# Optimization experiments

Hardware: AMD Instinct MI355X
Metric: run time of the kernel (lower is better)

Reference implementation:

```python
import jax, jax.numpy as jnp
from jax import lax
import numpy as np

MAXMAG = 10.0   # max_residue_magnitude
DG = 16         # deformable_groups
K = 9           # 3x3 kernel taps


def _conv(x, w, b):
    return lax.conv_general_dilated(x, w, (1, 1), 'SAME',
                                    dimension_numbers=('NCHW', 'OIHW', 'NCHW')) + b[None, :, None, None]


def _lrelu(v):
    return jnp.where(v >= 0, v, 0.1 * v)


def _sample(img, py, px):
    # img [C,H,W]; py,px [K,H,W] absolute sample coords; bilinear, zeros outside (torchvision semantics)
    H, W = img.shape[1], img.shape[2]
    y0 = jnp.floor(py)
    x0 = jnp.floor(px)
    wy1 = py - y0
    wx1 = px - x0

    def gather(yi, xi):
        valid = ((yi >= 0) & (yi < H) & (xi >= 0) & (xi < W)).astype(img.dtype)
        yc = jnp.clip(yi, 0, H - 1).astype(jnp.int32)
        xc = jnp.clip(xi, 0, W - 1).astype(jnp.int32)
        return img[:, yc, xc] * valid[None]  # [C,K,H,W]

    v00 = gather(y0, x0)
    v01 = gather(y0, x0 + 1)
    v10 = gather(y0 + 1, x0)
    v11 = gather(y0 + 1, x0 + 1)
    return (v00 * ((1 - wy1) * (1 - wx1))[None] + v01 * ((1 - wy1) * wx1)[None]
            + v10 * (wy1 * (1 - wx1))[None] + v11 * (wy1 * wx1)[None])


def setup_inputs() -> dict:
    key = jax.random.key(0)
    ks = jax.random.split(key, 12)
    N, CIN, COUT, H, W = 4, 128, 64, 96, 96
    f = lambda k, sh, s: jax.random.normal(k, sh, dtype=jnp.float32) * s
    return {
        'x': f(ks[0], (N, CIN, H, W), 1.0),
        'extra_feat': f(ks[1], (N, 3 * COUT, H, W), 1.0),
        'flow_1': f(ks[2], (N, 2, H, W), 2.0),
        'flow_2': f(ks[3], (N, 2, H, W), 2.0),
        'w_off0': f(ks[4], (COUT, 3 * COUT + 4, 3, 3), 0.02), 'b_off0': jnp.zeros((COUT,), jnp.float32),
        'w_off1': f(ks[5], (COUT, COUT, 3, 3), 0.04), 'b_off1': jnp.zeros((COUT,), jnp.float32),
        'w_off2': f(ks[6], (COUT, COUT, 3, 3), 0.04), 'b_off2': jnp.zeros((COUT,), jnp.float32),
        'w_off3': f(ks[7], (27 * DG, COUT, 3, 3), 0.02), 'b_off3': jnp.zeros((27 * DG,), jnp.float32),
        'w_dcn': f(ks[8], (COUT, CIN, 3, 3), 0.03), 'b_dcn': jnp.zeros((COUT,), jnp.float32),
    }


def reference(x, extra_feat, flow_1, flow_2, w_off0, b_off0, w_off1, b_off1,
              w_off2, b_off2, w_off3, b_off3, w_dcn, b_dcn):
    N, CIN, H, W = x.shape
    COUT = w_dcn.shape[0]
    Cg = CIN // DG
    # conv_offset stack on cat([extra_feat, flow_1, flow_2])
    feat = jnp.concatenate([extra_feat, flow_1, flow_2], axis=1)
    h = _lrelu(_conv(feat, w_off0, b_off0))
    h = _lrelu(_conv(h, w_off1, b_off1))
    h = _lrelu(_conv(h, w_off2, b_off2))
    out = _conv(h, w_off3, b_off3)                      # [N, 27*DG, H, W]
    o1, o2, mask = jnp.split(out, 3, axis=1)            # each [N, 9*DG, H, W]
    offs = MAXMAG * jnp.tanh(jnp.concatenate([o1, o2], axis=1))
    off1, off2 = jnp.split(offs, 2, axis=1)
    # flow.flip(1) -> (dy, dx); repeat interleaves over the 72 (tap) pairs
    off1 = off1 + jnp.tile(flow_1[:, ::-1], (1, off1.shape[1] // 2, 1, 1))
    off2 = off2 + jnp.tile(flow_2[:, ::-1], (1, off2.shape[1] // 2, 1, 1))
    # torchvision layout: channel c = g*2*K + 2*k + {y,x}; groups 0..7 <- off1, 8..15 <- off2
    off = jnp.concatenate([off1, off2], axis=1).reshape(N, DG, K, 2, H, W)
    m = jax.nn.sigmoid(mask).reshape(N, DG, K, H, W)
    # absolute sampling positions per tap
    kk = jnp.arange(K)
    ky = (kk // 3 - 1).astype(x.dtype)[:, None, None]
    kx = (kk % 3 - 1).astype(x.dtype)[:, None, None]
    gy = jnp.arange(H, dtype=x.dtype)[:, None]
    gx = jnp.arange(W, dtype=x.dtype)[None, :]
    py = off[:, :, :, 0] + ky + gy                      # [N,DG,K,H,W]
    px = off[:, :, :, 1] + kx + gx
    xg = x.reshape(N, DG, Cg, H, W)
    sampled = jax.vmap(jax.vmap(_sample))(xg, py, px)   # [N,DG,Cg,K,H,W]
    wg = w_dcn.reshape(COUT, DG, Cg, K)
    y = jnp.einsum('ngckhw,ogck->nohw', sampled * m[:, :, None], wg)
    return y + b_dcn[None, :, None, None]
```

## Files before the change

kernel.cpp:

```cpp
#include <hip/hip_runtime.h>
#include <math.h>

#define NB 4
#define HH 96
#define WW 96
#define HW (HH*WW)
#define NPIX (NB*HW)
#define C_IN 128
#define C_OUT 64
#define DGRP 16
#define CG 8

typedef short v8s __attribute__((ext_vector_type(8)));
typedef float v4f __attribute__((ext_vector_type(4)));
typedef unsigned short u16;
typedef unsigned int u32;

__device__ __forceinline__ u16 f2bf(float x) {
    u32 u = __float_as_uint(x);
    u32 r = (u + 0x7FFFu + ((u >> 16) & 1u)) >> 16;
    return (u16)r;
}
__device__ __forceinline__ float bf2f(u16 h) {
    return __uint_as_float(((u32)h) << 16);
}
__device__ __forceinline__ float lo_bf(u32 w) { return __uint_as_float(w << 16); }
__device__ __forceinline__ float hi_bf(u32 w) { return __uint_as_float(w & 0xFFFF0000u); }
__device__ __forceinline__ float ftanh(float x) {
    float e = __expf(2.0f * x);
    return 1.0f - 2.0f / (e + 1.0f);
}
__device__ __forceinline__ float fsigm(float x) {
    return 1.0f / (1.0f + __expf(-x));
}
__device__ __forceinline__ v8s u4_to_v8s(uint4 q) {
    union { uint4 q; v8s s; } u; u.q = q; return u.s;
}
__device__ __forceinline__ u32 cvtpk(float a, float b) {
    u32 r;
    asm("v_cvt_pk_bf16_f32 %0, %1, %2" : "=v"(r) : "v"(a), "v"(b));
    return r;
}
typedef __attribute__((address_space(1))) const char gch1;
typedef __attribute__((address_space(3))) char ch3;
__device__ __forceinline__ void gload16(const void* g, void* l) {
    __builtin_amdgcn_global_load_lds((gch1*)g, (ch3*)l, 16, 0, 0);
}

__global__ __launch_bounds__(256) void prep_catT(
    const float* __restrict__ ef, const float* __restrict__ f1,
    const float* __restrict__ f2, u16* __restrict__ catT)
{
    __shared__ float T[64][65];
    const int t   = threadIdx.x;
    const int p   = blockIdx.x * 64;
    const int ch0 = blockIdx.y * 64;
    const int n   = p / HW;
    const int rem = p - n * HW;
    const int px  = t & 63;
    const int wv  = t >> 6;
    #pragma unroll
    for (int kk = 0; kk < 16; ++kk) {
        int chl = wv * 16 + kk;
        int ch  = ch0 + chl;
        float v = 0.f;
        if (ch < 192)      v = ef[(size_t)(n * 192 + ch) * HW + rem + px];
        else if (ch < 194) v = f1[(size_t)(n * 2 + (ch - 192)) * HW + rem + px];
        else if (ch < 196) v = f2[(size_t)(n * 2 + (ch - 194)) * HW + rem + px];
        T[chl][px] = v;
    }
    __syncthreads();
    const int s = t & 7;
    #pragma unroll
    for (int it = 0; it < 2; ++it) {
        int pxo = (t >> 3) + it * 32;
        u32 w0 = (u32)f2bf(T[s*8+0][pxo]) | ((u32)f2bf(T[s*8+1][pxo]) << 16);
        u32 w1 = (u32)f2bf(T[s*8+2][pxo]) | ((u32)f2bf(T[s*8+3][pxo]) << 16);
        u32 w2 = (u32)f2bf(T[s*8+4][pxo]) | ((u32)f2bf(T[s*8+5][pxo]) << 16);
        u32 w3 = (u32)f2bf(T[s*8+6][pxo]) | ((u32)f2bf(T[s*8+7][pxo]) << 16);
        *(uint4*)&catT[((size_t)(p + pxo)) * 256 + ch0 + s * 8] = make_uint4(w0, w1, w2, w3);
    }
}

__global__ __launch_bounds__(256) void prep_xT(
    const float* __restrict__ x, u16* __restrict__ xT)
{
    __shared__ float T[64][65];
    const int t   = threadIdx.x;
    const int p   = blockIdx.x * 64;
    const int ch0 = blockIdx.y * 64;
    const int n   = p / HW;
    const int rem = p - n * HW;
    const int px  = t & 63;
    const int wv  = t >> 6;
    #pragma unroll
    for (int kk = 0; kk < 16; ++kk) {
        int chl = wv * 16 + kk;
        T[chl][px] = x[(size_t)(n * C_IN + ch0 + chl) * HW + rem + px];
    }
    __syncthreads();
    const int s = t & 7;
    #pragma unroll
    for (int it = 0; it < 2; ++it) {
        int pxo = (t >> 3) + it * 32;
        u32 w0 = (u32)f2bf(T[s*8+0][pxo]) | ((u32)f2bf(T[s*8+1][pxo]) << 16);
        u32 w1 = (u32)f2bf(T[s*8+2][pxo]) | ((u32)f2bf(T[s*8+3][pxo]) << 16);
        u32 w2 = (u32)f2bf(T[s*8+4][pxo]) | ((u32)f2bf(T[s*8+5][pxo]) << 16);
        u32 w3 = (u32)f2bf(T[s*8+6][pxo]) | ((u32)f2bf(T[s*8+7][pxo]) << 16);
        *(uint4*)&xT[((size_t)(ch0 / 8 + s) * NPIX + (p + pxo)) * 8] = make_uint4(w0, w1, w2, w3);
    }
}

__device__ __forceinline__ void pack_wf_one(
    const float* __restrict__ w, u16* __restrict__ wp,
    int Cout, int CoutPad, int CIN, int CIP, int idx)
{
    const int NKF = CIP / 32, NOG = CoutPad / 16;
    int c    = idx & 7;
    int ln   = (idx >> 3) & 63;
    int rest = idx >> 9;
    int og   = rest % NOG; rest /= NOG;
    int kfg  = rest % NKF;
    int tap  = rest / NKF;
    int l15 = ln & 15, lg = ln >> 4;
    int o  = og * 16 + l15;
    int ci = kfg * 32 + lg * 8 + c;
    float v = (o < Cout && ci < CIN) ? w[((size_t)o * CIN + ci) * 9 + tap] : 0.f;
    wp[idx] = f2bf(v);
}

__global__ __launch_bounds__(256) void pack_all(
    const float* __restrict__ w0, u16* __restrict__ w0p,
    const float* __restrict__ w1, u16* __restrict__ w1p,
    const float* __restrict__ w2, u16* __restrict__ w2p,
    const float* __restrict__ w3, u16* __restrict__ w3p,
    const float* __restrict__ wd, u16* __restrict__ wdf,
    uint4* __restrict__ zp)
{
    if (blockIdx.x == 0 && threadIdx.x < 32)
        zp[threadIdx.x] = make_uint4(0u, 0u, 0u, 0u);
    int idx = blockIdx.x * 256 + threadIdx.x;
    if (idx < 147456) { pack_wf_one(w0, w0p, 64, 64, 196, 256, idx); return; }
    idx -= 147456;
    if (idx < 36864)  { pack_wf_one(w1, w1p, 64, 64, 64, 64, idx); return; }
    idx -= 36864;
    if (idx < 36864)  { pack_wf_one(w2, w2p, 64, 64, 64, 64, idx); return; }
    idx -= 36864;
    if (idx < 258048) { pack_wf_one(w3, w3p, 432, 448, 64, 64, idx); return; }
    idx -= 258048;
    {
        int c  = idx & 7;
        int ln = (idx >> 3) & 63;
        int m  = (idx >> 9) & 3;
        int kk = idx >> 11;
        int l15 = ln & 15, lg = ln >> 4;
        int o = m * 16 + l15;
        int slot = kk * 4 + lg;
        int g = slot / 9, kt = slot - 9 * g;
        wdf[idx] = f2bf(wd[((size_t)(o * C_IN + g * CG + c)) * 9 + kt]);
    }
}

template<int CIP, int NCHUNK, int OST, bool LRELU, bool TOUT, int NOB>
__global__ __launch_bounds__(256) void conv_mfma(
    const u16* __restrict__ inT,
    const u16* __restrict__ wp,
    const float* __restrict__ bias,
    int CoutReal,
    u16* __restrict__ outT,
    u32* __restrict__ pairT,
    u16* __restrict__ maskT,
    const char* __restrict__ zpc)
{
    constexpr int COLS  = (NOB > 1) ? 100 : 50;
    constexpr int LTILE = 3 * COLS * 64;
    constexpr int LTILE_PAD = (NOB == 1) ? LTILE + 128 : LTILE;
    constexpr int LSZ   = (NCHUNK > 1) ? 2 * LTILE_PAD : LTILE_PAD;
    constexpr int NKF   = CIP / 32;
    constexpr int NOG   = OST / 16;
    __shared__ __align__(16) u16 L[LSZ];

    const int t   = threadIdx.x;
    const int tb  = blockIdx.x;
    const int row = (NOB > 1) ? tb : (tb >> 1);
    const int p0  = (NOB > 1) ? 0 : (tb & 1) * 48;
    const int n   = row / HH;
    const int h   = row - n * HH;
    const int ln  = t & 63;
    const int wv  = t >> 6;
    const int l15 = ln & 15;
    const int lg  = ln >> 4;

    auto stage = [&](int ch, int buf) {
        const int cb = ch * 64;
        const int NCOL = (NOB > 1) ? 98 : 50;
        const int NTASK = 3 * NCOL * 8;
        u16* Lb = &L[buf * LTILE_PAD];
        #pragma unroll
        for (int it = 0; it < (NTASK + 255) / 256; ++it) {
            int task = it * 256 + t;
            if (task < NTASK) {
                int s  = task & 7;
                int cl = task >> 3;
                int r3 = cl / NCOL;
                int c  = cl - r3 * NCOL;
                int yy = h + r3 - 1;
                int xx = p0 + c - 1;
                uint4 v = make_uint4(0u, 0u, 0u, 0u);
                if ((unsigned)yy < HH && (unsigned)xx < WW)
                    v = *(const uint4*)&inT[((size_t)(n * HW + yy * WW + xx)) * CIP + cb + s * 8];
                *(uint4*)&Lb[(r3 * COLS + c) * 64 + ((s ^ (c & 7)) * 8)] = v;
            }
        }
    };

    if constexpr (NOB == 1) {
        const char* inTc = (const char*)inT;
        auto mk = [&](int it) -> const char* {
            int task = it * 256 + t;
            if (task >= 1200) return zpc;
            int s  = task & 7;
            int cl = task >> 3;
            int r3 = cl / 50;
            int c  = cl - r3 * 50;
            int yy = h + r3 - 1;
            int xx = p0 + c - 1;
            bool v = ((unsigned)yy < HH) && ((unsigned)xx < WW);
            int sp = s ^ (c & 7);
            u32 off = ((u32)(n * HW + yy * WW + xx) * (u32)CIP + (u32)(sp * 8)) * 2u;
            return v ? inTc + off : zpc;
        };
        const char* pb0 = mk(0);
        const char* pb1 = mk(1);
        const char* pb2 = mk(2);
        const char* pb3 = mk(3);
        const char* pb4 = mk(4);

        auto gstage = [&](int ch, int buf) {
            u16* Lb = &L[buf * LTILE_PAD];
            const u32 cb2 = (u32)ch * 128u;
            gload16(pb0 + cb2, &Lb[(u32)(0 * 256 + t) * 8u]);
            gload16(pb1 + cb2, &Lb[(u32)(1 * 256 + t) * 8u]);
            gload16(pb2 + cb2, &Lb[(u32)(2 * 256 + t) * 8u]);
            gload16(pb3 + cb2, &Lb[(u32)(3 * 256 + t) * 8u]);
            if (4 * 256 + t < 1200)
                gload16(pb4 + cb2, &Lb[(u32)(4 * 256 + t) * 8u]);
        };

        v4f acc[3];
        #pragma unroll
        for (int i = 0; i < 3; ++i) acc[i] = (v4f){0.f, 0.f, 0.f, 0.f};

        gstage(0, 0);
        for (int ch = 0; ch < NCHUNK; ++ch) {
            __syncthreads();
            if (ch + 1 < NCHUNK) gstage(ch + 1, (ch + 1) & 1);
            const u16* Lb = &L[(ch & 1) * LTILE_PAD];
            #pragma unroll
            for (int tap = 0; tap < 9; ++tap) {
                const int ty = tap / 3, tx = tap - ty * 3;
                #pragma unroll
                for (int kf = 0; kf < 2; ++kf) {
                    v8s b = *(const v8s*)&wp[((((size_t)tap * NKF + (ch * 2 + kf)) * NOG + wv) * 64 + ln) * 8];
                    #pragma unroll
                    for (int fm = 0; fm < 3; ++fm) {
                        int c = fm * 16 + l15 + tx;
                        v8s a = *(const v8s*)&Lb[(ty * COLS + c) * 64 + (((kf * 4 + lg) ^ (c & 7)) * 8)];
                        acc[fm] = __builtin_amdgcn_mfma_f32_16x16x32_bf16(a, b, acc[fm], 0, 0, 0);
                    }
                }
            }
        }

        int o = wv * 16 + l15;
        float bv = (o < CoutReal) ? bias[o] : 0.f;
        #pragma unroll
        for (int fm = 0; fm < 3; ++fm) {
            #pragma unroll
            for (int r = 0; r < 4; ++r) {
                int px = p0 + fm * 16 + lg * 4 + r;
                float v = acc[fm][r] + bv;
                if (LRELU) v = (v >= 0.f) ? v : 0.1f * v;
                outT[((size_t)(n * HW + h * WW + px)) * OST + o] = f2bf(v);
            }
        }
    } else {
        stage(0, 0);
        __syncthreads();
        const size_t gpix = (size_t)n * HW + h * WW;
        const int ob_lo = blockIdx.y * 4;
        const int ob_hi = (ob_lo + 4 < NOB) ? ob_lo + 4 : NOB;

        for (int ob = ob_lo; ob < ob_hi; ++ob) {
            const int obase = ob * 64 + wv * 16;
            if (obase >= 432) continue;

            v4f acc[6];
            #pragma unroll
            for (int i = 0; i < 6; ++i) acc[i] = (v4f){0.f, 0.f, 0.f, 0.f};

            #pragma unroll
            for (int tap = 0; tap < 9; ++tap) {
                const int ty = tap / 3, tx = tap - ty * 3;
                #pragma unroll
                for (int kf = 0; kf < 2; ++kf) {
                    v8s bw = *(const v8s*)&wp[((((size_t)tap * NKF + kf) * NOG + (ob * 4 + wv)) * 64 + ln) * 8];
                    #pragma unroll
                    for (int fm = 0; fm < 6; ++fm) {
                        int c = fm * 16 + l15 + tx;
                        v8s a = *(const v8s*)&L[(ty * COLS + c) * 64 + (((kf * 4 + lg) ^ (c & 7)) * 8)];
                        acc[fm] = __builtin_amdgcn_mfma_f32_16x16x32_bf16(bw, a, acc[fm], 0, 0, 0);
                    }
                }
            }

            float bv[4];
            #pragma unroll
            for (int r = 0; r < 4; ++r) bv[r] = bias[obase + lg * 4 + r];

            if (obase < 288) {
                const int pr = (obase + lg * 4) >> 1;
                #pragma unroll
                for (int fm = 0; fm < 6; ++fm) {
                    const size_t pix = gpix + fm * 16 + l15;
                    u32 v0 = (u32)f2bf(acc[fm][0] + bv[0]) | ((u32)f2bf(acc[fm][1] + bv[1]) << 16);
                    u32 v1 = (u32)f2bf(acc[fm][2] + bv[2]) | ((u32)f2bf(acc[fm][3] + bv[3]) << 16);
                    pairT[(size_t)pr * NPIX + pix]       = v0;
                    pairT[(size_t)(pr + 1) * NPIX + pix] = v1;
                }
            } else {
                #pragma unroll
                for (int fm = 0; fm < 6; ++fm) {
                    const size_t pix = gpix + fm * 16 + l15;
                    #pragma unroll
                    for (int r = 0; r < 4; ++r) {
                        int mch = obase + lg * 4 + r - 288;
                        maskT[(size_t)mch * NPIX + pix] = f2bf(acc[fm][r] + bv[r]);
                    }
                }
            }
        }
    }
}

__global__ __launch_bounds__(384) void dcn_fused(
    const u16* __restrict__ xT,
    const float* __restrict__ f1,
    const float* __restrict__ f2,
    const u32*  __restrict__ pairT,
    const u16*  __restrict__ maskT,
    const u16*  __restrict__ wdf,
    const float* __restrict__ bdcn,
    float* __restrict__ y)
{
    __shared__ __align__(16) v4f R[2][4][128];

    const int t    = threadIdx.x;
    const int xb   = blockIdx.x;
    const int xw   = (xb & 7) * 144 + (xb >> 3);
    const int p0   = xw * 32;
    const int w6   = t >> 6;
    const int ks   = w6 >> 1;
    const int wvs  = w6 & 1;
    const int ln   = t & 63;
    const int l15  = ln & 15;
    const int lg   = ln >> 4;
    const int ts   = wvs * 64 + ln;
    const int n    = p0 / HW;
    const int rem0 = p0 - n * HW;
    const int p    = p0 + wvs * 16 + l15;
    const int rem  = rem0 + wvs * 16 + l15;
    const int h    = rem / WW;
    const int w    = rem - h * WW;

    const char* pTc = (const char*)pairT;
    const char* mTc = (const char*)maskT;
    const char* xTc = (const char*)xT;
    const u32 p4   = (u32)p << 2;
    const u32 p2   = (u32)p << 1;
    const u32 nb16 = (u32)(n * HW) << 4;

    const float f1yh = f1[(size_t)(n * 2 + 1) * HW + rem] + (float)h;
    const float f1xw = f1[(size_t)(n * 2 + 0) * HW + rem] + (float)w;
    const float f2yh = f2[(size_t)(n * 2 + 1) * HW + rem] + (float)h;
    const float f2xw = f2[(size_t)(n * 2 + 0) * HW + rem] + (float)w;

    auto scal = [&](int sl, u32& yx, float& mr) {
        yx = *(const u32*)(pTc + ((u32)sl * (u32)(NPIX * 4) + p4));
        mr = bf2f(*(const u16*)(mTc + ((u32)sl * (u32)(NPIX * 2) + p2)));
    };

    auto coords = [&](int sl, u32 yx, float mr,
                      uint4& q00, uint4& q01, uint4& q10, uint4& q11,
                      float& w00, float& w01, float& w10, float& w11) {
        const int g  = (sl * 57) >> 9;
        const int kt = sl - 9 * g;
        const int ky = (kt * 11) >> 5;
        const int kx = kt - 3 * ky;
        const float fy = (g < 8) ? f1yh : f2yh;
        const float fx = (g < 8) ? f1xw : f2xw;
        const float py  = 10.0f * ftanh(lo_bf(yx)) + (fy + (float)(ky - 1));
        const float pxx = 10.0f * ftanh(hi_bf(yx)) + (fx + (float)(kx - 1));
        const float m   = fsigm(mr);

        const float y0f = floorf(py), x0f = floorf(pxx);
        const int   iy0 = (int)y0f,   ix0 = (int)x0f;
        const float wy = py - y0f, wx = pxx - x0f;
        const bool v0y = ((unsigned)iy0 < HH);
        const bool v1y = ((unsigned)(iy0 + 1) < HH);
        const bool v0x = ((unsigned)ix0 < WW);
        const bool v1x = ((unsigned)(ix0 + 1) < WW);
        const float wy0m = (1.0f - wy) * m, wy1m = wy * m;
        w00 = (v0y && v0x) ? wy0m * (1.0f - wx) : 0.0f;
        w01 = (v0y && v1x) ? wy0m * wx          : 0.0f;
        w10 = (v1y && v0x) ? wy1m * (1.0f - wx) : 0.0f;
        w11 = (v1y && v1x) ? wy1m * wx          : 0.0f;

        const int iy0c = min(max(iy0, 0), HH - 1);
        const int iy1c = min(max(iy0 + 1, 0), HH - 1);
        const int ix0c = min(max(ix0, 0), WW - 1);
        const int ix1c = min(max(ix0 + 1, 0), WW - 1);
        const u32 gof = (u32)g * (u32)(NPIX * 16) + nb16;
        const u32 r0  = gof + (u32)iy0c * (u32)(WW * 16);
        const u32 r1  = gof + (u32)iy1c * (u32)(WW * 16);
        const u32 c0  = (u32)ix0c << 4;
        const u32 c1  = (u32)ix1c << 4;
        q00 = *(const uint4*)(xTc + (r0 + c0));
        q01 = *(const uint4*)(xTc + (r0 + c1));
        q10 = *(const uint4*)(xTc + (r1 + c0));
        q11 = *(const uint4*)(xTc + (r1 + c1));
    };

    auto blend = [&](const uint4& q00, const uint4& q01,
                     const uint4& q10, const uint4& q11,
                     float w00, float w01, float w10, float w11) -> v8s {
        u32 pv0 = cvtpk(
            w00*lo_bf(q00.x) + w01*lo_bf(q01.x) + w10*lo_bf(q10.x) + w11*lo_bf(q11.x),
            w00*hi_bf(q00.x) + w01*hi_bf(q01.x) + w10*hi_bf(q10.x) + w11*hi_bf(q11.x));
        u32 pv1 = cvtpk(
            w00*lo_bf(q00.y) + w01*lo_bf(q01.y) + w10*lo_bf(q10.y) + w11*lo_bf(q11.y),
            w00*hi_bf(q00.y) + w01*hi_bf(q01.y) + w10*hi_bf(q10.y) + w11*hi_bf(q11.y));
        u32 pv2 = cvtpk(
            w00*lo_bf(q00.z) + w01*lo_bf(q01.z) + w10*lo_bf(q10.z) + w11*lo_bf(q11.z),
            w00*hi_bf(q00.z) + w01*hi_bf(q01.z) + w10*hi_bf(q10.z) + w11*hi_bf(q11.z));
        u32 pv3 = cvtpk(
            w00*lo_bf(q00.w) + w01*lo_bf(q01.w) + w10*lo_bf(q10.w) + w11*lo_bf(q11.w),
            w00*hi_bf(q00.w) + w01*hi_bf(q01.w) + w10*hi_bf(q10.w) + w11*hi_bf(q11.w));
        return u4_to_v8s(make_uint4(pv0, pv1, pv2, pv3));
    };

    v4f acc[4];
    #pragma unroll
    for (int i = 0; i < 4; ++i) acc[i] = (v4f){0.f, 0.f, 0.f, 0.f};

    const int cc0 = ks * 12;
    const int sb  = cc0 * 4 + lg;
    const char* wb = (const char*)wdf + ((u32)cc0 << 12) + ((u32)ln << 4);

    uint4 qA00, qA01, qA10, qA11;  float wA00, wA01, wA10, wA11;
    uint4 qB00, qB01, qB10, qB11;  float wB00, wB01, wB10, wB11;
    u32 yxN; float mrN;

    {
        u32 yx; float mr;
        scal(sb, yx, mr);
        coords(sb, yx, mr, qA00, qA01, qA10, qA11, wA00, wA01, wA10, wA11);
        scal(sb + 4, yx, mr);
        coords(sb + 4, yx, mr, qB00, qB01, qB10, qB11, wB00, wB01, wB10, wB11);
        scal(sb + 8, yxN, mrN);
    }

    #pragma unroll 1
    for (int j = 0; j < 12; j += 2) {
        {
            const char* wj = wb + ((u32)j << 12);
            v8s aW0 = *(const v8s*)(wj);
            v8s aW1 = *(const v8s*)(wj + 1024);
            v8s aW2 = *(const v8s*)(wj + 2048);
            v8s aW3 = *(const v8s*)(wj + 3072);
            v8s bP = blend(qA00, qA01, qA10, qA11, wA00, wA01, wA10, wA11);
            acc[0] = __builtin_amdgcn_mfma_f32_16x16x32_bf16(bP, aW0, acc[0], 0, 0, 0);
            acc[1] = __builtin_amdgcn_mfma_f32_16x16x32_bf16(bP, aW1, acc[1], 0, 0, 0);
            acc[2] = __builtin_amdgcn_mfma_f32_16x16x32_bf16(bP, aW2, acc[2], 0, 0, 0);
            acc[3] = __builtin_amdgcn_mfma_f32_16x16x32_bf16(bP, aW3, acc[3], 0, 0, 0);
            if (j + 2 < 12)
                coords(sb + (j + 2) * 4, yxN, mrN,
                       qA00, qA01, qA10, qA11, wA00, wA01, wA10, wA11);
            if (j + 3 < 12) scal(sb + (j + 3) * 4, yxN, mrN);
        }
        {
            const char* wj = wb + ((u32)(j + 1) << 12);
            v8s aW0 = *(const v8s*)(wj);
            v8s aW1 = *(const v8s*)(wj + 1024);
            v8s aW2 = *(const v8s*)(wj + 2048);
            v8s aW3 = *(const v8s*)(wj + 3072);
            v8s bP = blend(qB00, qB01, qB10, qB11, wB00, wB01, wB10, wB11);
            acc[0] = __builtin_amdgcn_mfma_f32_16x16x32_bf16(bP, aW0, acc[0], 0, 0, 0);
            acc[1] = __builtin_amdgcn_mfma_f32_16x16x32_bf16(bP, aW1, acc[1], 0, 0, 0);
            acc[2] = __builtin_amdgcn_mfma_f32_16x16x32_bf16(bP, aW2, acc[2], 0, 0, 0);
            acc[3] = __builtin_amdgcn_mfma_f32_16x16x32_bf16(bP, aW3, acc[3], 0, 0, 0);
            if (j + 3 < 12)
                coords(sb + (j + 3) * 4, yxN, mrN,
                       qB00, qB01, qB10, qB11, wB00, wB01, wB10, wB11);
            if (j + 4 < 12) scal(sb + (j + 4) * 4, yxN, mrN);
        }
    }

    if (ks > 0) {
        #pragma unroll
        for (int m = 0; m < 4; ++m) R[ks - 1][m][ts] = acc[m];
    }
    __syncthreads();
    if (ks == 0) {
        #pragma unroll
        for (int m = 0; m < 4; ++m) {
            v4f s = acc[m];
            v4f r1 = R[0][m][ts];
            v4f r2 = R[1][m][ts];
            const int o = m * 16 + l15;
            const float bd = bdcn[o];
            const size_t idx = (size_t)(n * C_OUT + o) * HW + rem0 + wvs * 16 + lg * 4;
            *(float4*)&y[idx] = make_float4(s[0] + r1[0] + r2[0] + bd,
                                            s[1] + r1[1] + r2[1] + bd,
                                            s[2] + r1[2] + r2[2] + bd,
                                            s[3] + r1[3] + r2[3] + bd);
        }
    }
}

extern "C" void kernel_launch(void* const* d_in, const int* in_sizes, int n_in,
                              void* d_out, int out_size, void* d_ws, size_t ws_size,
                              hipStream_t stream) {
    const float* x  = (const float*)d_in[0];
    const float* ef = (const float*)d_in[1];
    const float* f1 = (const float*)d_in[2];
    const float* f2 = (const float*)d_in[3];
    const float* w0 = (const float*)d_in[4];
    const float* b0 = (const float*)d_in[5];
    const float* w1 = (const float*)d_in[6];
    const float* b1 = (const float*)d_in[7];
    const float* w2 = (const float*)d_in[8];
    const float* b2 = (const float*)d_in[9];
    const float* w3 = (const float*)d_in[10];
    const float* b3 = (const float*)d_in[11];
    const float* wd = (const float*)d_in[12];
    const float* bd = (const float*)d_in[13];
    float* y = (float*)d_out;
    char* wsb = (char*)d_ws;

    u16* catT  = (u16*)(wsb + 0);
    u16* h0T   = (u16*)(wsb + 18874368);
    u16* h1T   = (u16*)(wsb + 23592960);
    u16* h2T   = (u16*)(wsb + 28311552);
    u32* pairT = (u32*)(wsb + 33030144);
    u16* maskT = (u16*)(wsb + 54263808);
    u16* w0p   = (u16*)(wsb + 64880640);
    u16* w1p   = (u16*)(wsb + 65175552);
    u16* w2p   = (u16*)(wsb + 65249280);
    u16* w3p   = (u16*)(wsb + 65323008);
    u16* wdf   = (u16*)(wsb + 65839104);
    u16* xT    = (u16*)(wsb + 65986560);
    char* zp   = (wsb + 75423744);

    prep_catT<<<dim3(NPIX / 64, 4), 256, 0, stream>>>(ef, f1, f2, catT);
    prep_xT  <<<dim3(NPIX / 64, 2), 256, 0, stream>>>(x, xT);
    pack_all <<<dim3(552960 / 256), 256, 0, stream>>>(
        w0, w0p, w1, w1p, w2, w2p, w3, w3p, wd, wdf, (uint4*)zp);

    conv_mfma<256, 4, 64, true,  false, 1><<<dim3(768), 256, 0, stream>>>(
        catT, w0p, b0, 64, h0T, nullptr, nullptr, zp);
    conv_mfma< 64, 1, 64, true,  false, 1><<<dim3(768), 256, 0, stream>>>(
        h0T, w1p, b1, 64, h1T, nullptr, nullptr, zp);
    conv_mfma< 64, 1, 64, true,  false, 1><<<dim3(768), 256, 0, stream>>>(
        h1T, w2p, b2, 64, h2T, nullptr, nullptr, zp);
    conv_mfma< 64, 1, 448, false, true, 7><<<dim3(NB * HH, 2), 256, 0, stream>>>(
        h2T, w3p, b3, 432, nullptr, pairT, maskT, zp);

    dcn_fused<<<dim3(NPIX / 32), 384, 0, stream>>>(
        xT, f1, f2, pairT, maskT, wdf, bd, y);
}
```

Before: 133.7 us.

## Merge prep kernels, skip zero-padded K chunk, halve DCN block tile

Three prep kernels (activation transposes and weight packing) become one launch that picks its role from the block index, which removes two launches and their gaps. The first offset conv skips the final k-fragment whose input channels (224-255) are pure zero padding, saving MFMA and LDS reads. The fused deformable conv now handles 16 pixels per block with 192 threads instead of 32 pixels with 384, doubling the grid to raise occupancy and parallelism. The smaller blocks mean more blocks and reductions for the same work.

```diff
diff --git a/kernel.cpp b/kernel.cpp
--- a/kernel.cpp
+++ b/kernel.cpp
@@ -45,70 +45,6 @@
 typedef __attribute__((address_space(3))) char ch3;
 __device__ __forceinline__ void gload16(const void* g, void* l) {
     __builtin_amdgcn_global_load_lds((gch1*)g, (ch3*)l, 16, 0, 0);
-}
-
-__global__ __launch_bounds__(256) void prep_catT(
-    const float* __restrict__ ef, const float* __restrict__ f1,
-    const float* __restrict__ f2, u16* __restrict__ catT)
-{
-    __shared__ float T[64][65];
-    const int t   = threadIdx.x;
-    const int p   = blockIdx.x * 64;
-    const int ch0 = blockIdx.y * 64;
-    const int n   = p / HW;
-    const int rem = p - n * HW;
-    const int px  = t & 63;
-    const int wv  = t >> 6;
-    #pragma unroll
-    for (int kk = 0; kk < 16; ++kk) {
-        int chl = wv * 16 + kk;
-        int ch  = ch0 + chl;
-        float v = 0.f;
-        if (ch < 192)      v = ef[(size_t)(n * 192 + ch) * HW + rem + px];
-        else if (ch < 194) v = f1[(size_t)(n * 2 + (ch - 192)) * HW + rem + px];
-        else if (ch < 196) v = f2[(size_t)(n * 2 + (ch - 194)) * HW + rem + px];
-        T[chl][px] = v;
-    }
-    __syncthreads();
-    const int s = t & 7;
-    #pragma unroll
-    for (int it = 0; it < 2; ++it) {
-        int pxo = (t >> 3) + it * 32;
-        u32 w0 = (u32)f2bf(T[s*8+0][pxo]) | ((u32)f2bf(T[s*8+1][pxo]) << 16);
-        u32 w1 = (u32)f2bf(T[s*8+2][pxo]) | ((u32)f2bf(T[s*8+3][pxo]) << 16);
-        u32 w2 = (u32)f2bf(T[s*8+4][pxo]) | ((u32)f2bf(T[s*8+5][pxo]) << 16);
-        u32 w3 = (u32)f2bf(T[s*8+6][pxo]) | ((u32)f2bf(T[s*8+7][pxo]) << 16);
-        *(uint4*)&catT[((size_t)(p + pxo)) * 256 + ch0 + s * 8] = make_uint4(w0, w1, w2, w3);
-    }
-}
-
-__global__ __launch_bounds__(256) void prep_xT(
-    const float* __restrict__ x, u16* __restrict__ xT)
-{
-    __shared__ float T[64][65];
-    const int t   = threadIdx.x;
-    const int p   = blockIdx.x * 64;
-    const int ch0 = blockIdx.y * 64;
-    const int n   = p / HW;
-    const int rem = p - n * HW;
-    const int px  = t & 63;
-    const int wv  = t >> 6;
-    #pragma unroll
-    for (int kk = 0; kk < 16; ++kk) {
-        int chl = wv * 16 + kk;
-        T[chl][px] = x[(size_t)(n * C_IN + ch0 + chl) * HW + rem + px];
-    }
-    __syncthreads();
-    const int s = t & 7;
-    #pragma unroll
-    for (int it = 0; it < 2; ++it) {
-        int pxo = (t >> 3) + it * 32;
-        u32 w0 = (u32)f2bf(T[s*8+0][pxo]) | ((u32)f2bf(T[s*8+1][pxo]) << 16);
-        u32 w1 = (u32)f2bf(T[s*8+2][pxo]) | ((u32)f2bf(T[s*8+3][pxo]) << 16);
-        u32 w2 = (u32)f2bf(T[s*8+4][pxo]) | ((u32)f2bf(T[s*8+5][pxo]) << 16);
-        u32 w3 = (u32)f2bf(T[s*8+6][pxo]) | ((u32)f2bf(T[s*8+7][pxo]) << 16);
-        *(uint4*)&xT[((size_t)(ch0 / 8 + s) * NPIX + (p + pxo)) * 8] = make_uint4(w0, w1, w2, w3);
-    }
 }
 
 __device__ __forceinline__ void pack_wf_one(
@@ -129,7 +65,10 @@
     wp[idx] = f2bf(v);
 }
 
-__global__ __launch_bounds__(256) void pack_all(
+__global__ __launch_bounds__(256) void prep_all(
+    const float* __restrict__ ef, const float* __restrict__ f1,
+    const float* __restrict__ f2, const float* __restrict__ x,
+    u16* __restrict__ catT, u16* __restrict__ xT,
     const float* __restrict__ w0, u16* __restrict__ w0p,
     const float* __restrict__ w1, u16* __restrict__ w1p,
     const float* __restrict__ w2, u16* __restrict__ w2p,
@@ -137,9 +76,72 @@
     const float* __restrict__ wd, u16* __restrict__ wdf,
     uint4* __restrict__ zp)
 {
-    if (blockIdx.x == 0 && threadIdx.x < 32)
-        zp[threadIdx.x] = make_uint4(0u, 0u, 0u, 0u);
-    int idx = blockIdx.x * 256 + threadIdx.x;
+    __shared__ float T[64][65];
+    const int t = threadIdx.x;
+    int bid = blockIdx.x;
+
+    if (bid < 2304) {
+        const int by  = bid / 576, bx = bid - by * 576;
+        const int p   = bx * 64;
+        const int ch0 = by * 64;
+        const int n   = p / HW;
+        const int rem = p - n * HW;
+        const int px  = t & 63;
+        const int wv  = t >> 6;
+        #pragma unroll
+        for (int kk = 0; kk < 16; ++kk) {
+            int chl = wv * 16 + kk;
+            int ch  = ch0 + chl;
+            float v = 0.f;
+            if (ch < 192)      v = ef[(size_t)(n * 192 + ch) * HW + rem + px];
+            else if (ch < 194) v = f1[(size_t)(n * 2 + (ch - 192)) * HW + rem + px];
+            else if (ch < 196) v = f2[(size_t)(n * 2 + (ch - 194)) * HW + rem + px];
+            T[chl][px] = v;
+        }
+        __syncthreads();
+        const int s = t & 7;
+        #pragma unroll
+        for (int it = 0; it < 2; ++it) {
+            int pxo = (t >> 3) + it * 32;
+            u32 q0 = (u32)f2bf(T[s*8+0][pxo]) | ((u32)f2bf(T[s*8+1][pxo]) << 16);
+            u32 q1 = (u32)f2bf(T[s*8+2][pxo]) | ((u32)f2bf(T[s*8+3][pxo]) << 16);
+            u32 q2 = (u32)f2bf(T[s*8+4][pxo]) | ((u32)f2bf(T[s*8+5][pxo]) << 16);
+            u32 q3 = (u32)f2bf(T[s*8+6][pxo]) | ((u32)f2bf(T[s*8+7][pxo]) << 16);
+            *(uint4*)&catT[((size_t)(p + pxo)) * 256 + ch0 + s * 8] = make_uint4(q0, q1, q2, q3);
+        }
+        return;
+    }
+    bid -= 2304;
+    if (bid < 1152) {
+        const int by  = bid / 576, bx = bid - by * 576;
+        const int p   = bx * 64;
+        const int ch0 = by * 64;
+        const int n   = p / HW;
+        const int rem = p - n * HW;
+        const int px  = t & 63;
+        const int wv  = t >> 6;
+        #pragma unroll
+        for (int kk = 0; kk < 16; ++kk) {
+            int chl = wv * 16 + kk;
+            T[chl][px] = x[(size_t)(n * C_IN + ch0 + chl) * HW + rem + px];
+        }
+        __syncthreads();
+        const int s = t & 7;
+        #pragma unroll
+        for (int it = 0; it < 2; ++it) {
+            int pxo = (t >> 3) + it * 32;
+            u32 q0 = (u32)f2bf(T[s*8+0][pxo]) | ((u32)f2bf(T[s*8+1][pxo]) << 16);
+            u32 q1 = (u32)f2bf(T[s*8+2][pxo]) | ((u32)f2bf(T[s*8+3][pxo]) << 16);
+            u32 q2 = (u32)f2bf(T[s*8+4][pxo]) | ((u32)f2bf(T[s*8+5][pxo]) << 16);
+            u32 q3 = (u32)f2bf(T[s*8+6][pxo]) | ((u32)f2bf(T[s*8+7][pxo]) << 16);
+            *(uint4*)&xT[((size_t)(ch0 / 8 + s) * NPIX + (p + pxo)) * 8] = make_uint4(q0, q1, q2, q3);
+        }
+        return;
+    }
+    bid -= 1152;
+    if (bid == 0 && t < 32)
+        zp[t] = make_uint4(0u, 0u, 0u, 0u);
+    int idx = bid * 256 + t;
     if (idx < 147456) { pack_wf_one(w0, w0p, 64, 64, 196, 256, idx); return; }
     idx -= 147456;
     if (idx < 36864)  { pack_wf_one(w1, w1p, 64, 64, 64, 64, idx); return; }
@@ -261,6 +263,7 @@
                 const int ty = tap / 3, tx = tap - ty * 3;
                 #pragma unroll
                 for (int kf = 0; kf < 2; ++kf) {
+                    if (CIP == 256 && ch == 3 && kf == 1) continue;
                     v8s b = *(const v8s*)&wp[((((size_t)tap * NKF + (ch * 2 + kf)) * NOG + wv) * 64 + ln) * 8];
                     #pragma unroll
                     for (int fm = 0; fm < 3; ++fm) {
@@ -343,7 +346,7 @@
     }
 }
 
-__global__ __launch_bounds__(384) void dcn_fused(
+__global__ __launch_bounds__(192) void dcn_fused(
     const u16* __restrict__ xT,
     const float* __restrict__ f1,
     const float* __restrict__ f2,
@@ -353,23 +356,20 @@
     const float* __restrict__ bdcn,
     float* __restrict__ y)
 {
-    __shared__ __align__(16) v4f R[2][4][128];
+    __shared__ __align__(16) v4f R[2][4][64];
 
     const int t    = threadIdx.x;
     const int xb   = blockIdx.x;
-    const int xw   = (xb & 7) * 144 + (xb >> 3);
-    const int p0   = xw * 32;
-    const int w6   = t >> 6;
-    const int ks   = w6 >> 1;
-    const int wvs  = w6 & 1;
+    const int xw   = (xb & 7) * 288 + (xb >> 3);
+    const int p0   = xw * 16;
+    const int ks   = t >> 6;
     const int ln   = t & 63;
     const int l15  = ln & 15;
     const int lg   = ln >> 4;
-    const int ts   = wvs * 64 + ln;
     const int n    = p0 / HW;
     const int rem0 = p0 - n * HW;
-    const int p    = p0 + wvs * 16 + l15;
-    const int rem  = rem0 + wvs * 16 + l15;
+    const int p    = p0 + l15;
+    const int rem  = rem0 + l15;
     const int h    = rem / WW;
     const int w    = rem - h * WW;
 
@@ -508,18 +508,18 @@
 
     if (ks > 0) {
         #pragma unroll
-        for (int m = 0; m < 4; ++m) R[ks - 1][m][ts] = acc[m];
+        for (int m = 0; m < 4; ++m) R[ks - 1][m][ln] = acc[m];
     }
     __syncthreads();
     if (ks == 0) {
         #pragma unroll
         for (int m = 0; m < 4; ++m) {
             v4f s = acc[m];
-            v4f r1 = R[0][m][ts];
-            v4f r2 = R[1][m][ts];
+            v4f r1 = R[0][m][ln];
+            v4f r2 = R[1][m][ln];
             const int o = m * 16 + l15;
             const float bd = bdcn[o];
-            const size_t idx = (size_t)(n * C_OUT + o) * HW + rem0 + wvs * 16 + lg * 4;
+            const size_t idx = (size_t)(n * C_OUT + o) * HW + rem0 + lg * 4;
             *(float4*)&y[idx] = make_float4(s[0] + r1[0] + r2[0] + bd,
                                             s[1] + r1[1] + r2[1] + bd,
                                             s[2] + r1[2] + r2[2] + bd,
@@ -562,9 +562,8 @@
     u16* xT    = (u16*)(wsb + 65986560);
     char* zp   = (wsb + 75423744);
 
-    prep_catT<<<dim3(NPIX / 64, 4), 256, 0, stream>>>(ef, f1, f2, catT);
-    prep_xT  <<<dim3(NPIX / 64, 2), 256, 0, stream>>>(x, xT);
-    pack_all <<<dim3(552960 / 256), 256, 0, stream>>>(
+    prep_all<<<dim3(5616), 256, 0, stream>>>(
+        ef, f1, f2, x, catT, xT,
         w0, w0p, w1, w1p, w2, w2p, w3, w3p, wd, wdf, (uint4*)zp);
 
     conv_mfma<256, 4, 64, true,  false, 1><<<dim3(768), 256, 0, stream>>>(
@@ -576,6 +575,6 @@
     conv_mfma< 64, 1, 448, false, true, 7><<<dim3(NB * HH, 2), 256, 0, stream>>>(
         h2T, w3p, b3, 432, nullptr, pairT, maskT, zp);
 
-    dcn_fused<<<dim3(NPIX / 32), 384, 0, stream>>>(
+    dcn_fused<<<dim3(NPIX / 16), 192, 0, stream>>>(
         xT, f1, f2, pairT, maskT, wdf, bd, y);
 }
```

Measured after the change: 117.3 us. 1.14x faster.
